# Performance work log

Measured on AMD Instinct MI355X. Metric: run time of the kernel, lower is better.

## Reference

```python
import jax, jax.numpy as jnp
import numpy as np
from jax import lax

EPS = 1e-5  # flax BatchNorm default epsilon


def _conv(x, w, b, padding='SAME'):
    y = lax.conv_general_dilated(x, w, (1, 1), padding,
                                 dimension_numbers=('NHWC', 'HWIO', 'NHWC'))
    return y + b


def _maxpool(x, window, strides):
    return lax.reduce_window(x, -jnp.inf, lax.max,
                             (1,) + window + (1,), (1,) + strides + (1,), 'SAME')


def _bn_train(x, scale, bias):
    # training-mode BatchNorm: batch statistics over N,H,W
    m = x.mean(axis=(0, 1, 2))
    v = x.var(axis=(0, 1, 2))
    return (x - m) * lax.rsqrt(v + EPS) * scale + bias


def _lstm(x, wx, wh, b, carry, reverse):
    # x: (B, T, D); flax LSTMCell gate order i, f, g, o; bias lives on the
    # hidden dense in flax but is an equivalent single additive term here.
    xs = jnp.swapaxes(x @ wx + b, 0, 1)  # (T, B, 4H), input GEMM hoisted out of scan

    def step(ch, xt):
        c, h = ch
        g = xt + h @ wh
        i, f, gg, o = jnp.split(g, 4, axis=-1)
        c = jax.nn.sigmoid(f) * c + jax.nn.sigmoid(i) * jnp.tanh(gg)
        h = jax.nn.sigmoid(o) * jnp.tanh(c)
        return (c, h), h

    carry, ys = lax.scan(step, carry, xs, reverse=reverse)
    return carry, jnp.swapaxes(ys, 0, 1)  # (B, T, H)


def _forward(x, conv1_w, conv1_b, conv2_w, conv2_b, conv3_w, conv3_b, bn1_s, bn1_b,
             conv4_w, conv4_b, bn2_s, bn2_b, conv5_w, conv5_b, bn3_s, bn3_b,
             conv6_w, conv6_b, bn4_s, bn4_b, conv7_w, conv7_b, bn5_s, bn5_b,
             wq, bq, wk, bk, wv, bv,
             l1f_wx, l1f_wh, l1f_b, l1r_wx, l1r_wh, l1r_b,
             l2f_wx, l2f_wh, l2f_b, l2r_wx, l2r_wh, l2r_b, wo, bo):
    x = jax.nn.relu(_conv(x, conv1_w, conv1_b))
    x = _maxpool(x, (2, 2), (2, 2))
    x = jax.nn.relu(_conv(x, conv2_w, conv2_b))
    x = _maxpool(x, (2, 2), (2, 2))
    x = jax.nn.relu(_bn_train(_conv(x, conv3_w, conv3_b), bn1_s, bn1_b))
    x = jax.nn.relu(_bn_train(_conv(x, conv4_w, conv4_b), bn2_s, bn2_b))
    x = _maxpool(x, (2, 2), (1, 2))
    x = jax.nn.relu(_bn_train(_conv(x, conv5_w, conv5_b), bn3_s, bn3_b))
    x = jax.nn.relu(_bn_train(_conv(x, conv6_w, conv6_b), bn4_s, bn4_b))
    x = _maxpool(x, (2, 2), (1, 2))
    x = jax.nn.relu(_bn_train(_conv(x, conv7_w, conv7_b, padding='VALID'), bn5_s, bn5_b))
    B = x.shape[0]
    x = x.reshape(B, x.shape[1], -1)  # (B, T=H', W'*512); seq axis is height
    q = x @ wq + bq
    k = x @ wk + bk
    v = x @ wv + bv
    qk = jax.nn.softmax(jnp.einsum('btk,bsk->bts', q, k) / 32.0, axis=-1)
    x = jnp.einsum('btk,bts->bsk', v, qk)
    # stack 1: reverse LSTM deliberately starts from forward's FINAL carry (as in source)
    carry = (jnp.zeros((B, 256), x.dtype), jnp.zeros((B, 256), x.dtype))
    carry, y1 = _lstm(x, l1f_wx, l1f_wh, l1f_b, carry, reverse=False)
    carry, y2 = _lstm(x, l1r_wx, l1r_wh, l1r_b, carry, reverse=True)
    x1 = jnp.concatenate([y1, y2], axis=-1)
    # stack 2
    carry = (jnp.zeros((B, 512), x.dtype), jnp.zeros((B, 512), x.dtype))
    carry, y2b = _lstm(x1, l2f_wx, l2f_wh, l2f_b, carry, reverse=False)
    carry, y3 = _lstm(x1, l2r_wx, l2r_wh, l2r_b, carry, reverse=True)
    x = jnp.concatenate([y3, y2b], axis=-1)
    return x @ wo + bo


def setup_inputs() -> dict:
    key = jax.random.key(0)
    ks = iter(jax.random.split(key, 64))

    def cw(kh, kw, ci, co):
        return jax.random.normal(next(ks), (kh, kw, ci, co), jnp.float32) / np.float32(np.sqrt(kh * kw * ci))

    def dw(i, o):
        return jax.random.normal(next(ks), (i, o), jnp.float32) / np.float32(np.sqrt(i))

    z = lambda *s: jnp.zeros(s, jnp.float32)
    ones = lambda *s: jnp.ones(s, jnp.float32)
    class_nums = 1000
    d_in = 15 * 512  # W'=15 after conv stack, 512 channels
    inp = {
        'x': jax.random.normal(next(ks), (32, 64, 256, 3), jnp.float32),
        'conv1_w': cw(3, 3, 3, 64), 'conv1_b': z(64),
        'conv2_w': cw(3, 3, 64, 128), 'conv2_b': z(128),
        'conv3_w': cw(3, 3, 128, 256), 'conv3_b': z(256), 'bn1_s': ones(256), 'bn1_b': z(256),
        'conv4_w': cw(3, 3, 256, 256), 'conv4_b': z(256), 'bn2_s': ones(256), 'bn2_b': z(256),
        'conv5_w': cw(3, 3, 256, 512), 'conv5_b': z(512), 'bn3_s': ones(512), 'bn3_b': z(512),
        'conv6_w': cw(3, 3, 512, 512), 'conv6_b': z(512), 'bn4_s': ones(512), 'bn4_b': z(512),
        'conv7_w': cw(2, 2, 512, 512), 'conv7_b': z(512), 'bn5_s': ones(512), 'bn5_b': z(512),
        'wq': dw(d_in, 512), 'bq': z(512),
        'wk': dw(d_in, 512), 'bk': z(512),
        'wv': dw(d_in, 512), 'bv': z(512),
        'l1f_wx': dw(512, 4 * 256), 'l1f_wh': dw(256, 4 * 256), 'l1f_b': z(4 * 256),
        'l1r_wx': dw(512, 4 * 256), 'l1r_wh': dw(256, 4 * 256), 'l1r_b': z(4 * 256),
        'l2f_wx': dw(512, 4 * 512), 'l2f_wh': dw(512, 4 * 512), 'l2f_b': z(4 * 512),
        'l2r_wx': dw(512, 4 * 512), 'l2r_wh': dw(512, 4 * 512), 'l2r_b': z(4 * 512),
        'wo': dw(1024, class_nums), 'bo': z(class_nums),
    }
    return inp


def reference(x, conv1_w, conv1_b, conv2_w, conv2_b, conv3_w, conv3_b, bn1_s, bn1_b,
              conv4_w, conv4_b, bn2_s, bn2_b, conv5_w, conv5_b, bn3_s, bn3_b,
              conv6_w, conv6_b, bn4_s, bn4_b, conv7_w, conv7_b, bn5_s, bn5_b,
              wq, bq, wk, bk, wv, bv,
              l1f_wx, l1f_wh, l1f_b, l1r_wx, l1r_wh, l1r_b,
              l2f_wx, l2f_wh, l2f_b, l2r_wx, l2r_wh, l2r_b, wo, bo):
    return _forward(x, conv1_w, conv1_b, conv2_w, conv2_b, conv3_w, conv3_b, bn1_s, bn1_b,
                    conv4_w, conv4_b, bn2_s, bn2_b, conv5_w, conv5_b, bn3_s, bn3_b,
                    conv6_w, conv6_b, bn4_s, bn4_b, conv7_w, conv7_b, bn5_s, bn5_b,
                    wq, bq, wk, bk, wv, bv,
                    l1f_wx, l1f_wh, l1f_b, l1r_wx, l1r_wh, l1r_b,
                    l2f_wx, l2f_wh, l2f_b, l2r_wx, l2r_wh, l2r_b, wo, bo)
```

## Files before the change

### kernel.cpp

```cpp
#include <hip/hip_runtime.h>
#include <math.h>

#define DIV_UP(a,b) (((a)+(b)-1)/(b))

typedef _Float16 half_t;
typedef _Float16 half8 __attribute__((ext_vector_type(8)));
typedef float f32x4 __attribute__((ext_vector_type(4)));

#define FLAG_RELU   1
#define FLAG_OUTF32 2
#define FLAG_SPLITK 4
#define FLAG_ATOMIC 8
#define FLAG_BNSUMS 16

#define GLDS16(src, dst) \
  __builtin_amdgcn_global_load_lds((const __attribute__((address_space(1))) void*)(src), \
                                   (__attribute__((address_space(3))) void*)(dst), 16, 0, 0)

__device__ __forceinline__ float fsig_(float x){ return 1.0f/(1.0f+__expf(-x)); }
__device__ __forceinline__ float ftanh_(float x){
  float ax = fabsf(x);
  float e = __expf(-2.0f*ax);
  float t = (1.0f - e)/(1.0f + e);
  return copysignf(t, x);
}

#define NTP 18
struct TpAll {
  const float* src[NTP];
  half_t* dst[NTP];
  int K[NTP];
  int N[NTP];
  int prefix[NTP+1];
};

__global__ __launch_bounds__(256) void transpose_cvt_all_kernel(TpAll a)
{
  __shared__ float tile[32][33];
  int bid = blockIdx.x;
  int z = 0;
  while (bid >= a.prefix[z+1]) ++z;
  int local = bid - a.prefix[z];
  const float* w = a.src[z];
  half_t* wT = a.dst[z];
  int K = a.K[z], N = a.N[z];
  int tilesX = (N + 31) >> 5;
  int nt = (local % tilesX) * 32;
  int kt = (local / tilesX) * 32;
  int tx = threadIdx.x & 31, ty = threadIdx.x >> 5;
  #pragma unroll
  for (int r = 0; r < 4; ++r) {
    int k = kt + ty + r*8, n = nt + tx;
    tile[ty + r*8][tx] = (k < K && n < N) ? w[(long)k*N + n] : 0.f;
  }
  __syncthreads();
  #pragma unroll
  for (int r = 0; r < 4; ++r) {
    int n = nt + ty + r*8, k = kt + tx;
    if (n < N && k < K) wT[(long)n*K + k] = (half_t)tile[tx][ty + r*8];
  }
}

__global__ __launch_bounds__(256) void conv1_kernel(
    const float* __restrict__ x, const float* __restrict__ w,
    const float* __restrict__ bias, half_t* __restrict__ out)
{
  __shared__ float xs[3][258*3];
  int nb = blockIdx.x;
  int n = nb >> 6, ho = nb & 63;
  int tid = threadIdx.x;
  int co = tid & 63;
  float wreg[27];
  #pragma unroll
  for (int k = 0; k < 27; ++k) wreg[k] = w[k*64 + co];
  float bco = bias[co];
  for (int i = tid; i < 3*258*3; i += 256) {
    int row = i / (258*3); int rem = i % (258*3);
    int col = rem / 3;     int ci  = rem % 3;
    int ih = ho - 1 + row; int iw = col - 1;
    float v = 0.f;
    if (ih >= 0 && ih < 64 && iw >= 0 && iw < 256)
      v = x[(((long)n*64 + ih)*256 + iw)*3 + ci];
    xs[row][col*3 + ci] = v;
  }
  __syncthreads();
  int wave = tid >> 6;
  for (int p = 0; p < 64; ++p) {
    int wo = wave*64 + p;
    float acc = bco;
    #pragma unroll
    for (int kh = 0; kh < 3; ++kh)
      #pragma unroll
      for (int kw = 0; kw < 3; ++kw)
        #pragma unroll
        for (int ci = 0; ci < 3; ++ci)
          acc = fmaf(xs[kh][(wo+kw)*3 + ci], wreg[(kh*3+kw)*3 + ci], acc);
    acc = fmaxf(acc, 0.f);
    out[(((long)n*64 + ho)*256 + wo)*64 + co] = (half_t)acc;
  }
}

struct GOut { const half_t* wT; const float* bias; void* out; };

__global__ __launch_bounds__(256) void mfma_conv_kernel(
    const half_t* __restrict__ x, GOut g0, GOut g1, GOut g2,
    const half_t* __restrict__ zbuf, float* __restrict__ bns,
    int N,int H,int W,int Ci,int Ho,int Wo,int Co,
    int KH,int KW,int padH,int padW,
    int M,int K,int flags,int splitS)
{
  GOut g;
  int ciBeg = 0, ciEnd = Ci;
  if (flags & FLAG_SPLITK) {
    g = g0;
    int span = Ci / splitS;
    ciBeg = blockIdx.z * span;
    ciEnd = ciBeg + span;
  } else {
    g = (blockIdx.z == 0) ? g0 : (blockIdx.z == 1 ? g1 : g2);
  }
  const half_t* __restrict__ wT = g.wT;
  __shared__ half_t As[2][128*64];
  __shared__ half_t Bs[2][128*64];
  int tid = threadIdx.x;

  int nbx = gridDim.x, nby = gridDim.y;
  int total = nbx * nby;
  int flat = blockIdx.y * nbx + blockIdx.x;
  int q = total >> 3, r = total & 7;
  int xcd = flat & 7;
  int j = flat >> 3;
  int w = xcd * q + (xcd < r ? xcd : r) + j;
  int m0 = (w / nbx) * 128, n0 = (w % nbx) * 128;

  int wave = tid >> 6, lane = tid & 63;
  int l15 = lane & 15, quad = lane >> 4;
  int x7 = lane & 7;
  int wm = (wave & 1) * 64, wn = (wave >> 1) * 64;

  int rSub = tid >> 3;
  int colHalf = (((tid & 7) ^ (rSub & 7))) * 8;

  int ho_[4], wo_[4], ni_[4]; bool av_[4];
  #pragma unroll
  for (int i = 0; i < 4; ++i) {
    int m = m0 + i*32 + rSub;
    av_[i] = m < M;
    int mm = av_[i] ? m : 0;
    wo_[i] = mm % Wo; int t2 = mm / Wo;
    ho_[i] = t2 % Ho; ni_[i] = t2 / Ho;
  }
  const half_t* bBase[4];
  #pragma unroll
  for (int i = 0; i < 4; ++i) {
    int n = n0 + i*32 + rSub;
    bBase[i] = (n < Co) ? (wT + (long)n*K + colHalf) : nullptr;
  }

  int pch0 = ((quad)     ^ x7) * 8;
  int pch1 = ((4 + quad) ^ x7) * 8;

  f32x4 acc[4][4];
  #pragma unroll
  for (int i = 0; i < 4; ++i)
    #pragma unroll
    for (int j2 = 0; j2 < 4; ++j2)
      acc[i][j2] = (f32x4){0.f, 0.f, 0.f, 0.f};

  int NT = ((ciEnd - ciBeg) >> 6) * KH * KW;
  int skh = 0, skw = 0, sci = ciBeg;
  long sAOff[4]; bool sAval[4];
  auto recompA = [&]() {
    #pragma unroll
    for (int i = 0; i < 4; ++i) {
      int ih = ho_[i] - padH + skh, iw = wo_[i] - padW + skw;
      bool ok = av_[i] && ih >= 0 && ih < H && iw >= 0 && iw < W;
      sAval[i] = ok;
      sAOff[i] = ok ? ((((long)ni_[i]*H + ih)*W + iw)*(long)Ci + colHalf) : 0;
    }
  };
  recompA();
  auto stage = [&](int b) {
    int kgS = (skh*KW + skw)*Ci + sci;
    #pragma unroll
    for (int i = 0; i < 4; ++i) {
      const half_t* sa = sAval[i] ? (x + sAOff[i] + sci) : zbuf;
      GLDS16(sa, &As[b][i*2048 + wave*512]);
      const half_t* sb = bBase[i] ? (bBase[i] + kgS) : zbuf;
      GLDS16(sb, &Bs[b][i*2048 + wave*512]);
    }
  };
  auto advance = [&]() {
    sci += 64;
    if (sci == ciEnd) {
      sci = ciBeg; ++skw;
      if (skw == KW) { skw = 0; ++skh; }
      recompA();
    }
  };

  stage(0); advance();
  __syncthreads();

  for (int kt = 0; kt < NT; ++kt) {
    int p = kt & 1;
    if (kt + 1 < NT) { stage(p ^ 1); advance(); }
    {
      half8 af[4], bf[4];
      #pragma unroll
      for (int i = 0; i < 4; ++i)
        af[i] = *reinterpret_cast<half8*>(&As[p][(wm + i*16 + l15)*64 + pch0]);
      #pragma unroll
      for (int j2 = 0; j2 < 4; ++j2)
        bf[j2] = *reinterpret_cast<half8*>(&Bs[p][(wn + j2*16 + l15)*64 + pch0]);
      #pragma unroll
      for (int i = 0; i < 4; ++i)
        #pragma unroll
        for (int j2 = 0; j2 < 4; ++j2)
          acc[i][j2] = __builtin_amdgcn_mfma_f32_16x16x32_f16(af[i], bf[j2], acc[i][j2], 0, 0, 0);
    }
    {
      half8 af[4], bf[4];
      #pragma unroll
      for (int i = 0; i < 4; ++i)
        af[i] = *reinterpret_cast<half8*>(&As[p][(wm + i*16 + l15)*64 + pch1]);
      #pragma unroll
      for (int j2 = 0; j2 < 4; ++j2)
        bf[j2] = *reinterpret_cast<half8*>(&Bs[p][(wn + j2*16 + l15)*64 + pch1]);
      #pragma unroll
      for (int i = 0; i < 4; ++i)
        #pragma unroll
        for (int j2 = 0; j2 < 4; ++j2)
          acc[i][j2] = __builtin_amdgcn_mfma_f32_16x16x32_f16(af[i], bf[j2], acc[i][j2], 0, 0, 0);
    }
    __syncthreads();
  }

  if (flags & FLAG_BNSUMS) {
    float* red = (float*)As;
    #pragma unroll
    for (int j2 = 0; j2 < 4; ++j2) {
      int n = n0 + wn + j2*16 + l15;
      float bv = g.bias[n];
      float s = 0.f, qq = 0.f;
      #pragma unroll
      for (int i = 0; i < 4; ++i)
        #pragma unroll
        for (int rr = 0; rr < 4; ++rr) {
          int m = m0 + wm + i*16 + quad*4 + rr;
          if (m < M) { float v = acc[i][j2][rr] + bv; s += v; qq += v*v; }
        }
      int idx = ((((wave*4 + quad)*16 + l15)*4) + j2)*2;
      red[idx] = s; red[idx+1] = qq;
    }
    __syncthreads();
    if (tid < 128) {
      int hi = tid >> 6;
      int jj = (tid >> 4) & 3, ll = tid & 15;
      float s = 0.f, qq = 0.f;
      #pragma unroll
      for (int w2 = 0; w2 < 2; ++w2)
        #pragma unroll
        for (int qd = 0; qd < 4; ++qd) {
          int idx = (((((hi*2 + w2)*4 + qd)*16 + ll)*4) + jj)*2;
          s += red[idx]; qq += red[idx+1];
        }
      int n = n0 + tid;
      atomicAdd(&bns[n], s);
      atomicAdd(&bns[Co + n], qq);
    }
  }

  #pragma unroll
  for (int i = 0; i < 4; ++i) {
    #pragma unroll
    for (int rr = 0; rr < 4; ++rr) {
      int m = m0 + wm + i*16 + quad*4 + rr;
      if (m >= M) continue;
      #pragma unroll
      for (int j2 = 0; j2 < 4; ++j2) {
        int n = n0 + wn + j2*16 + l15;
        if (n >= Co) continue;
        if (flags & FLAG_ATOMIC) {
          atomicAdd(&((float*)g.out)[(long)m*Co + n], acc[i][j2][rr]);
        } else {
          float v = acc[i][j2][rr] + g.bias[n];
          if (flags & FLAG_RELU) v = fmaxf(v, 0.f);
          if (flags & FLAG_OUTF32) ((float*)g.out)[(long)m*Co + n] = v;
          else ((half_t*)g.out)[(long)m*Co + n] = (half_t)v;
        }
      }
    }
  }
}

__global__ __launch_bounds__(256) void maxpool8_kernel(
    const half_t* __restrict__ x, half_t* __restrict__ out,
    int N,int H,int W,int C,int Ho,int Wo,int sH,int sW)
{
  int C8 = C >> 3;
  long idx = (long)blockIdx.x*256 + threadIdx.x;
  long total8 = (long)N*Ho*Wo*C8;
  if (idx >= total8) return;
  int cb = (int)(idx % C8);
  long pix = idx / C8;
  int wo = (int)(pix % Wo); long t2 = pix / Wo;
  int ho = (int)(t2 % Ho); int n = (int)(t2 / Ho);
  int c = cb * 8;
  float m[8];
  #pragma unroll
  for (int e = 0; e < 8; ++e) m[e] = -INFINITY;
  for (int i = 0; i < 2; ++i) {
    int ih = ho*sH + i;
    if (ih >= H) continue;
    for (int j = 0; j < 2; ++j) {
      int iw = wo*sW + j;
      if (iw >= W) continue;
      half8 v = *reinterpret_cast<const half8*>(x + (((long)n*H + ih)*W + iw)*C + c);
      #pragma unroll
      for (int e = 0; e < 8; ++e) m[e] = fmaxf(m[e], (float)v[e]);
    }
  }
  half8 o;
  #pragma unroll
  for (int e = 0; e < 8; ++e) o[e] = (half_t)m[e];
  *reinterpret_cast<half8*>(out + idx*8) = o;
}

__global__ __launch_bounds__(256) void bn_apply_relu8_kernel(
    half_t* __restrict__ x, const float* __restrict__ sums,
    const float* __restrict__ scale, const float* __restrict__ bias,
    long total8, int C, float invN)
{
  long idx = (long)blockIdx.x*256 + threadIdx.x;
  if (idx >= total8) return;
  int c = (int)((idx*8) % C);
  half8 v = *reinterpret_cast<half8*>(x + idx*8);
  half8 o;
  #pragma unroll
  for (int e = 0; e < 8; ++e) {
    float mean = sums[c+e] * invN;
    float var  = sums[C + c+e] * invN - mean*mean;
    float rstd = rsqrtf(var + 1e-5f);
    float y = ((float)v[e] - mean) * rstd * scale[c+e] + bias[c+e];
    o[e] = (half_t)fmaxf(y, 0.0f);
  }
  *reinterpret_cast<half8*>(x + idx*8) = o;
}

__global__ __launch_bounds__(256) void bn_pool8_kernel(
    const half_t* __restrict__ x, half_t* __restrict__ out,
    const float* __restrict__ sums, const float* __restrict__ scale,
    const float* __restrict__ bias,
    int N,int H,int W,int C,int Ho,int Wo,int sH,int sW, float invN)
{
  int C8 = C >> 3;
  long idx = (long)blockIdx.x*256 + threadIdx.x;
  long total8 = (long)N*Ho*Wo*C8;
  if (idx >= total8) return;
  int cb = (int)(idx % C8);
  long pix = idx / C8;
  int wo = (int)(pix % Wo); long t2 = pix / Wo;
  int ho = (int)(t2 % Ho); int n = (int)(t2 / Ho);
  int c = cb * 8;
  float mean[8], rs[8], bb[8];
  #pragma unroll
  for (int e = 0; e < 8; ++e) {
    mean[e] = sums[c+e] * invN;
    float var = sums[C + c+e] * invN - mean[e]*mean[e];
    rs[e] = rsqrtf(var + 1e-5f) * scale[c+e];
    bb[e] = bias[c+e];
  }
  float m[8];
  #pragma unroll
  for (int e = 0; e < 8; ++e) m[e] = -INFINITY;
  for (int i = 0; i < 2; ++i) {
    int ih = ho*sH + i;
    if (ih >= H) continue;
    for (int j = 0; j < 2; ++j) {
      int iw = wo*sW + j;
      if (iw >= W) continue;
      half8 v = *reinterpret_cast<const half8*>(x + (((long)n*H + ih)*W + iw)*C + c);
      #pragma unroll
      for (int e = 0; e < 8; ++e) {
        float y = fmaxf(((float)v[e] - mean[e]) * rs[e] + bb[e], 0.f);
        m[e] = fmaxf(m[e], y);
      }
    }
  }
  half8 o;
  #pragma unroll
  for (int e = 0; e < 8; ++e) o[e] = (half_t)m[e];
  *reinterpret_cast<half8*>(out + idx*8) = o;
}

__global__ __launch_bounds__(256) void bias_fill_kernel(
    float* __restrict__ out, const float* __restrict__ b0,
    const float* __restrict__ b1, const float* __restrict__ b2, int total)
{
  int idx = blockIdx.x*256 + threadIdx.x;
  if (idx >= total) return;
  int n = idx % 1536;
  float v = (n < 512) ? b0[n] : (n < 1024 ? b1[n-512] : b2[n-1024]);
  out[idx] = v;
}

__global__ __launch_bounds__(256) void attention_kernel(
    const float* __restrict__ qkv, half_t* __restrict__ out,
    int T, int D, int ld)
{
  int b = blockIdx.x;
  int tid = threadIdx.x;
  __shared__ float P[15][16];
  if (tid < T*T) {
    int t = tid / T, s = tid % T;
    const float* qp = qkv + ((long)b*T + t)*ld;
    const float* kp = qkv + ((long)b*T + s)*ld + 512;
    float acc = 0.f;
    for (int d = 0; d < D; d += 4) {
      float4 qv = *reinterpret_cast<const float4*>(qp + d);
      float4 kv = *reinterpret_cast<const float4*>(kp + d);
      acc += qv.x*kv.x + qv.y*kv.y + qv.z*kv.z + qv.w*kv.w;
    }
    P[t][s] = acc * (1.0f/32.0f);
  }
  __syncthreads();
  if (tid < T) {
    float mx = -INFINITY;
    for (int s = 0; s < T; ++s) mx = fmaxf(mx, P[tid][s]);
    float sum = 0.f;
    for (int s = 0; s < T; ++s) { float e = expf(P[tid][s] - mx); P[tid][s] = e; sum += e; }
    float inv = 1.0f / sum;
    for (int s = 0; s < T; ++s) P[tid][s] *= inv;
  }
  __syncthreads();
  for (int idx = tid; idx < T*D; idx += 256) {
    int s = idx / D, kk2 = idx % D;
    float acc = 0.f;
    #pragma unroll
    for (int t = 0; t < 15; ++t)
      acc += qkv[((long)b*T + t)*ld + 1024 + kk2] * P[t][s];
    out[((long)b*T + s)*D + kk2] = (half_t)acc;
  }
}

#define MAXK 512
#define HSROW (MAXK + 8)

template<int N64, int HLOG>
__device__ __forceinline__ void stage_h(
    const unsigned long long* __restrict__ src, half_t (*hs)[HSROW], int tid)
{
  unsigned long long tmp[N64];
  #pragma unroll
  for (int u = 0; u < N64; ++u)
    tmp[u] = __hip_atomic_load(src + tid + u*256, __ATOMIC_RELAXED, __HIP_MEMORY_SCOPE_AGENT);
  #pragma unroll
  for (int u = 0; u < N64; ++u) {
    int idx = tid + u*256;
    int row = idx >> (HLOG - 2);
    int col = (idx & ((1 << (HLOG - 2)) - 1)) * 4;
    *reinterpret_cast<unsigned long long*>(&hs[row][col]) = tmp[u];
  }
}

template<int H>
__global__ __launch_bounds__(256, 1) void lstm_persistent_kernel(
    const float* __restrict__ preF, const float* __restrict__ preR,
    const half_t* __restrict__ whTF, const half_t* __restrict__ whTR,
    half_t* __restrict__ hbuf, half_t* __restrict__ y,
    int* __restrict__ flags, int nblk,
    int ystride, int yoffF, int yoffR)
{
  constexpr int KI = H / 32;
  __shared__ half_t hs[32][HSROW];
  __shared__ float gates[32][133];
  int tid = threadIdx.x;
  int jb0 = blockIdx.x * 32;
  int lane = tid & 63, wave = tid >> 6;
  int l15 = lane & 15, quad = lane >> 4;
  int bb = tid >> 3;
  int jj0 = (tid & 7) * 4;
  constexpr int H4 = 4 * H;

  float cst[4] = {0.f, 0.f, 0.f, 0.f};
  half8 wreg[2][KI];

  auto loadw = [&](const half_t* __restrict__ whT) {
    #pragma unroll
    for (int f = 0; f < 2; ++f) {
      const half_t* wp = whT + (long)(wave*H + jb0 + f*16 + l15)*H + quad*8;
      #pragma unroll
      for (int i = 0; i < KI; ++i)
        wreg[f][i] = *reinterpret_cast<const half8*>(wp + i*32);
    }
  };

  auto loadpv = [&](int s, float (&pv)[16]) {
    const float* pr = (s < 15) ? preF : preR;
    int t = (s < 15) ? s : 29 - s;
    const float* pp = pr + (long)(bb*15 + t)*H4 + jb0 + jj0;
    #pragma unroll
    for (int g = 0; g < 4; ++g) {
      f32x4 v = *reinterpret_cast<const f32x4*>(pp + g*H);
      pv[g*4+0] = v[0]; pv[g*4+1] = v[1]; pv[g*4+2] = v[2]; pv[g*4+3] = v[3];
    }
  };

  loadw(whTF);
  float pv[16];
  loadpv(0, pv);

  for (int s = 0; s < 30; ++s) {
    if (s == 15) loadw(whTR);
    int t = (s < 15) ? s : 29 - s;
    int yoff = (s < 15) ? yoffF : yoffR;

    const unsigned long long* hsrc =
        (const unsigned long long*)(hbuf + (long)(s & 1) * 32 * H);
    if constexpr (H == 512) stage_h<16, 9>(hsrc, hs, tid);
    else                    stage_h<8, 8>(hsrc, hs, tid);
    __syncthreads();

    f32x4 acc00 = {0.f,0.f,0.f,0.f}, acc10 = {0.f,0.f,0.f,0.f};
    f32x4 acc01 = {0.f,0.f,0.f,0.f}, acc11 = {0.f,0.f,0.f,0.f};
    #pragma unroll
    for (int i = 0; i < KI; ++i) {
      half8 a0 = *reinterpret_cast<half8*>(&hs[l15][i*32 + quad*8]);
      half8 a1 = *reinterpret_cast<half8*>(&hs[16 + l15][i*32 + quad*8]);
      acc00 = __builtin_amdgcn_mfma_f32_16x16x32_f16(a0, wreg[0][i], acc00, 0, 0, 0);
      acc10 = __builtin_amdgcn_mfma_f32_16x16x32_f16(a1, wreg[0][i], acc10, 0, 0, 0);
      acc01 = __builtin_amdgcn_mfma_f32_16x16x32_f16(a0, wreg[1][i], acc01, 0, 0, 0);
      acc11 = __builtin_amdgcn_mfma_f32_16x16x32_f16(a1, wreg[1][i], acc11, 0, 0, 0);
    }
    #pragma unroll
    for (int r = 0; r < 4; ++r) {
      gates[quad*4 + r][wave*32 + l15]           = acc00[r];
      gates[16 + quad*4 + r][wave*32 + l15]      = acc10[r];
      gates[quad*4 + r][wave*32 + 16 + l15]      = acc01[r];
      gates[16 + quad*4 + r][wave*32 + 16 + l15] = acc11[r];
    }
    __syncthreads();

    unsigned long long hpack;
    {
      half_t hn[4];
      #pragma unroll
      for (int p = 0; p < 4; ++p) {
        int j = jj0 + p;
        float gi = pv[p]      + gates[bb][j];
        float gf = pv[4 + p]  + gates[bb][32 + j];
        float gg = pv[8 + p]  + gates[bb][64 + j];
        float go = pv[12 + p] + gates[bb][96 + j];
        gi = fsig_(gi); gf = fsig_(gf); gg = ftanh_(gg); go = fsig_(go);
        float cn = gf * cst[p] + gi * gg;
        cst[p] = cn;
        hn[p] = (half_t)(go * ftanh_(cn));
      }
      hpack = *reinterpret_cast<unsigned long long*>(hn);
      half_t* hdst = hbuf + (long)((s + 1) & 1) * 32 * H;
      __hip_atomic_store((unsigned long long*)(hdst + (long)bb*H + jb0 + jj0), hpack,
                         __ATOMIC_RELAXED, __HIP_MEMORY_SCOPE_AGENT);
    }

    if (s < 29) {
      __syncthreads();
      if (tid == 0)
        __hip_atomic_store(&flags[blockIdx.x], s + 1,
                           __ATOMIC_RELAXED, __HIP_MEMORY_SCOPE_AGENT);
      *reinterpret_cast<unsigned long long*>(
          &y[(long)(bb*15 + t)*ystride + yoff + jb0 + jj0]) = hpack;
      loadpv(s + 1, pv);
      if (tid < 64) {
        int target = s + 1;
        for (;;) {
          int vv = (tid < nblk)
            ? __hip_atomic_load(&flags[tid], __ATOMIC_RELAXED, __HIP_MEMORY_SCOPE_AGENT)
            : target;
          if (__all(vv >= target)) break;
        }
      }
      __syncthreads();
    } else {
      *reinterpret_cast<unsigned long long*>(
          &y[(long)(bb*15 + t)*ystride + yoff + jb0 + jj0]) = hpack;
    }
  }
}

extern "C" void kernel_launch(void* const* d_in, const int* in_sizes, int n_in,
                              void* d_out, int out_size, void* d_ws, size_t ws_size,
                              hipStream_t stream)
{
  const float* x       = (const float*)d_in[0];
  const float* c1w     = (const float*)d_in[1];  const float* c1b = (const float*)d_in[2];
  const float* c2w     = (const float*)d_in[3];  const float* c2b = (const float*)d_in[4];
  const float* c3w     = (const float*)d_in[5];  const float* c3b = (const float*)d_in[6];
  const float* bn1s    = (const float*)d_in[7];  const float* bn1b = (const float*)d_in[8];
  const float* c4w     = (const float*)d_in[9];  const float* c4b = (const float*)d_in[10];
  const float* bn2s    = (const float*)d_in[11]; const float* bn2b = (const float*)d_in[12];
  const float* c5w     = (const float*)d_in[13]; const float* c5b = (const float*)d_in[14];
  const float* bn3s    = (const float*)d_in[15]; const float* bn3b = (const float*)d_in[16];
  const float* c6w     = (const float*)d_in[17]; const float* c6b = (const float*)d_in[18];
  const float* bn4s    = (const float*)d_in[19]; const float* bn4b = (const float*)d_in[20];
  const float* c7w     = (const float*)d_in[21]; const float* c7b = (const float*)d_in[22];
  const float* bn5s    = (const float*)d_in[23]; const float* bn5b = (const float*)d_in[24];
  const float* wq      = (const float*)d_in[25]; const float* bq = (const float*)d_in[26];
  const float* wk      = (const float*)d_in[27]; const float* bk = (const float*)d_in[28];
  const float* wv      = (const float*)d_in[29]; const float* bv = (const float*)d_in[30];
  const float* l1f_wx  = (const float*)d_in[31]; const float* l1f_wh = (const float*)d_in[32]; const float* l1f_b = (const float*)d_in[33];
  const float* l1r_wx  = (const float*)d_in[34]; const float* l1r_wh = (const float*)d_in[35]; const float* l1r_b = (const float*)d_in[36];
  const float* l2f_wx  = (const float*)d_in[37]; const float* l2f_wh = (const float*)d_in[38]; const float* l2f_b = (const float*)d_in[39];
  const float* l2r_wx  = (const float*)d_in[40]; const float* l2r_wh = (const float*)d_in[41]; const float* l2r_b = (const float*)d_in[42];
  const float* wo      = (const float*)d_in[43]; const float* bo = (const float*)d_in[44];
  float* outp = (float*)d_out;

  char* base = (char*)d_ws;
  half_t* actA = (half_t*)base;
  half_t* actB = (half_t*)(base + 67108864);
  half_t* wtA  = (half_t*)(base + 100663296);
  float*  f32a = (float*)(base + 143687680);
  half_t* h16a = (half_t*)(base + 158736384);

  half_t* wt2  = wtA;
  half_t* wt3  = wtA + 73728;
  half_t* wt4  = wtA + 368640;
  half_t* wt5  = wtA + 958464;
  half_t* wt6  = wtA + 2138112;
  half_t* wt7  = wtA + 4497408;
  half_t* wtq  = wtA + 5545984;
  half_t* wtk  = wtA + 9478144;
  half_t* wtv  = wtA + 13410304;
  half_t* wt1f = wtA + 17342464;
  half_t* wt1r = wtA + 17866752;
  half_t* wt2f = wtA + 18391040;
  half_t* wt2r = wtA + 19439616;
  half_t* wto  = wtA + 20488192;

  float* qkvbuf = f32a;
  float* pre1f = f32a + 737280;
  float* pre1r = f32a + 1228800;
  float* pre2f = f32a + 1720320;
  float* pre2r = f32a + 2703360;

  half_t* ao  = h16a;
  half_t* x1  = h16a + 245760;
  half_t* x2  = h16a + 491520;
  half_t* hb1 = h16a + 983040;
  half_t* hb2 = hb1 + 16384;
  int*    flags1 = (int*)(hb2 + 32768);
  int*    flags2 = flags1 + 512;
  half_t* zbuf   = (half_t*)(flags2 + 512);
  float*  bnz    = (float*)(zbuf + 32);

  half_t* whT1f = (half_t*)(base + 160849920);
  half_t* whT1r = (half_t*)(base + 161374208);
  half_t* whT2f = (half_t*)(base + 161898496);
  half_t* whT2r = (half_t*)(base + 163995648);

  auto convm = [&](const half_t* in, const half_t* wt, const float* b, void* out,
                   int N,int H,int W,int Ci,int Ho,int Wo,int Co,
                   int KH,int KW,int pH,int pW,int flags, float* bns){
    int M = N*Ho*Wo, K = KH*KW*Ci;
    dim3 grid(DIV_UP(Co,128), DIV_UP(M,128), 1);
    GOut g{wt, b, out};
    mfma_conv_kernel<<<grid,256,0,stream>>>(in,g,g,g,zbuf,bns,N,H,W,Ci,Ho,Wo,Co,
                                            KH,KW,pH,pW,M,K,flags,1);
  };
  auto gemm3 = [&](const half_t* A, GOut g0, GOut g1, GOut g2, int nz,
                   int M, int Nn, int K, int flags, int splitS){
    dim3 grid(DIV_UP(Nn,128), DIV_UP(M,128), nz);
    mfma_conv_kernel<<<grid,256,0,stream>>>(A,g0,g1,g2,zbuf,bnz,M,1,1,K,1,1,Nn,
                                            1,1,0,0,M,K,flags,splitS);
  };
  auto pool = [&](const half_t* in, half_t* out, int N,int H,int W,int C,
                  int Ho,int Wo,int sH,int sW){
    long total8 = (long)N*Ho*Wo*(C/8);
    maxpool8_kernel<<<(int)DIV_UP(total8,256),256,0,stream>>>(in,out,N,H,W,C,Ho,Wo,sH,sW);
  };
  auto bnApply = [&](half_t* buf, long nPix, int C, const float* s, const float* b,
                     float* sums){
    long total8 = nPix * C / 8;
    bn_apply_relu8_kernel<<<(int)DIV_UP(total8,256),256,0,stream>>>(buf, sums, s, b, total8, C, 1.0f/(float)nPix);
  };
  auto bnPool = [&](const half_t* in, half_t* out, int N,int H,int W,int C,
                    int Ho,int Wo,int sH,int sW, long nPix,
                    const float* s, const float* b, float* sums){
    long total8 = (long)N*Ho*Wo*(C/8);
    bn_pool8_kernel<<<(int)DIV_UP(total8,256),256,0,stream>>>(
        in,out,sums,s,b,N,H,W,C,Ho,Wo,sH,sW,1.0f/(float)nPix);
  };

  hipMemsetAsync(hb1, 0, 143424, stream);

  {
    TpAll tp;
    const float* srcs[NTP] = {c2w,c3w,c4w,c5w,c6w,c7w,wq,wk,wv,l1f_wx,l1r_wx,l2f_wx,l2r_wx,wo,
                              l1f_wh,l1r_wh,l2f_wh,l2r_wh};
    half_t* dsts[NTP] = {wt2,wt3,wt4,wt5,wt6,wt7,wtq,wtk,wtv,wt1f,wt1r,wt2f,wt2r,wto,
                         whT1f,whT1r,whT2f,whT2r};
    int Ks[NTP] = {576,1152,2304,2304,4608,2048,7680,7680,7680,512,512,512,512,1024,
                   256,256,512,512};
    int Ns[NTP] = {128,256,256,512,512,512,512,512,512,1024,1024,2048,2048,1000,
                   1024,1024,2048,2048};
    int acc = 0;
    for (int i = 0; i < NTP; ++i) {
      tp.src[i] = srcs[i]; tp.dst[i] = dsts[i]; tp.K[i] = Ks[i]; tp.N[i] = Ns[i];
      tp.prefix[i] = acc;
      acc += DIV_UP(Ks[i],32) * DIV_UP(Ns[i],32);
    }
    tp.prefix[NTP] = acc;
    transpose_cvt_all_kernel<<<acc,256,0,stream>>>(tp);
  }

  conv1_kernel<<<2048,256,0,stream>>>(x, c1w, c1b, actA);
  pool(actA, actB, 32,64,256,64,  32,128, 2,2);
  convm(actB, wt2, c2b, actA, 32,32,128,64,  32,128,128, 3,3,1,1, FLAG_RELU, bnz);
  pool(actA, actB, 32,32,128,128, 16,64, 2,2);
  convm(actB, wt3, c3b, actA, 32,16,64,128,  16,64,256,  3,3,1,1, FLAG_BNSUMS, bnz);
  bnApply(actA, 32768, 256, bn1s, bn1b, bnz);
  convm(actA, wt4, c4b, actB, 32,16,64,256,  16,64,256,  3,3,1,1, FLAG_BNSUMS, bnz + 2048);
  bnPool(actB, actA, 32,16,64,256, 16,32, 1,2, 32768, bn2s, bn2b, bnz + 2048);
  convm(actA, wt5, c5b, actB, 32,16,32,256,  16,32,512,  3,3,1,1, FLAG_BNSUMS, bnz + 4096);
  bnApply(actB, 16384, 512, bn3s, bn3b, bnz + 4096);
  convm(actB, wt6, c6b, actA, 32,16,32,512,  16,32,512,  3,3,1,1, FLAG_BNSUMS, bnz + 6144);
  bnPool(actA, actB, 32,16,32,512, 16,16, 1,2, 16384, bn4s, bn4b, bnz + 6144);
  convm(actB, wt7, c7b, actA, 32,16,16,512,  15,15,512,  2,2,0,0, FLAG_BNSUMS, bnz + 8192);
  bnApply(actA, 7200, 512, bn5s, bn5b, bnz + 8192);

  bias_fill_kernel<<<DIV_UP(480*1536,256),256,0,stream>>>(qkvbuf, bq, bk, bv, 480*1536);
  gemm3(actA, GOut{wtq, nullptr, qkvbuf}, GOut{wtq, nullptr, qkvbuf},
        GOut{wtq, nullptr, qkvbuf}, 4, 480, 1536, 7680, FLAG_SPLITK|FLAG_ATOMIC, 4);
  attention_kernel<<<32,256,0,stream>>>(qkvbuf, ao, 15, 512, 1536);

  gemm3(ao, GOut{wt1f, l1f_b, pre1f}, GOut{wt1r, l1r_b, pre1r},
        GOut{wt1r, l1r_b, pre1r}, 2, 480, 1024, 512, FLAG_OUTF32, 1);
  lstm_persistent_kernel<256><<<8,256,0,stream>>>(
      pre1f, pre1r, whT1f, whT1r, hb1, x1, flags1, 8, 512, 0, 256);

  gemm3(x1, GOut{wt2f, l2f_b, pre2f}, GOut{wt2r, l2r_b, pre2r},
        GOut{wt2r, l2r_b, pre2r}, 2, 480, 2048, 512, FLAG_OUTF32, 1);
  lstm_persistent_kernel<512><<<16,256,0,stream>>>(
      pre2f, pre2r, whT2f, whT2r, hb2, x2, flags2, 16, 1024, 512, 0);

  gemm3(x2, GOut{wto, bo, outp}, GOut{wto, bo, outp}, GOut{wto, bo, outp}, 1,
        480, 1000, 1024, FLAG_OUTF32, 1);
}
```

Measured before the change: 1.041 ms.

## Read LSTM hidden state directly from global, spin per-wave, drop register weights

The persistent LSTM kernel no longer stages the shared hidden state into LDS or keeps recurrent weights in registers. Each wave now spins on the block flags itself at the top of the step, then reads h fragments straight from global memory with atomic loads and reloads weight fragments every step. This removes a block barrier and the LDS staging pass from the serial critical path. In exchange it adds global and L2 traffic for both h and weights on every timestep, and the relaxed-ordering synchronisation becomes subtler.

```diff
diff --git a/kernel.cpp b/kernel.cpp
--- a/kernel.cpp
+++ b/kernel.cpp
@@ -444,26 +444,6 @@
   }
 }
 
-#define MAXK 512
-#define HSROW (MAXK + 8)
-
-template<int N64, int HLOG>
-__device__ __forceinline__ void stage_h(
-    const unsigned long long* __restrict__ src, half_t (*hs)[HSROW], int tid)
-{
-  unsigned long long tmp[N64];
-  #pragma unroll
-  for (int u = 0; u < N64; ++u)
-    tmp[u] = __hip_atomic_load(src + tid + u*256, __ATOMIC_RELAXED, __HIP_MEMORY_SCOPE_AGENT);
-  #pragma unroll
-  for (int u = 0; u < N64; ++u) {
-    int idx = tid + u*256;
-    int row = idx >> (HLOG - 2);
-    int col = (idx & ((1 << (HLOG - 2)) - 1)) * 4;
-    *reinterpret_cast<unsigned long long*>(&hs[row][col]) = tmp[u];
-  }
-}
-
 template<int H>
 __global__ __launch_bounds__(256, 1) void lstm_persistent_kernel(
     const float* __restrict__ preF, const float* __restrict__ preR,
@@ -473,7 +453,6 @@
     int ystride, int yoffF, int yoffR)
 {
   constexpr int KI = H / 32;
-  __shared__ half_t hs[32][HSROW];
   __shared__ float gates[32][133];
   int tid = threadIdx.x;
   int jb0 = blockIdx.x * 32;
@@ -484,17 +463,11 @@
   constexpr int H4 = 4 * H;
 
   float cst[4] = {0.f, 0.f, 0.f, 0.f};
-  half8 wreg[2][KI];
-
-  auto loadw = [&](const half_t* __restrict__ whT) {
-    #pragma unroll
-    for (int f = 0; f < 2; ++f) {
-      const half_t* wp = whT + (long)(wave*H + jb0 + f*16 + l15)*H + quad*8;
-      #pragma unroll
-      for (int i = 0; i < KI; ++i)
-        wreg[f][i] = *reinterpret_cast<const half8*>(wp + i*32);
-    }
-  };
+
+  int o0 = l15 * (H >> 2) + quad * 2;
+  int o1 = (16 + l15) * (H >> 2) + quad * 2;
+
+  const half_t* wB = whTF;
 
   auto loadpv = [&](int s, float (&pv)[16]) {
     const float* pr = (s < 15) ? preF : preR;
@@ -507,31 +480,41 @@
     }
   };
 
-  loadw(whTF);
   float pv[16];
   loadpv(0, pv);
 
   for (int s = 0; s < 30; ++s) {
-    if (s == 15) loadw(whTR);
+    if (s == 15) wB = whTR;
     int t = (s < 15) ? s : 29 - s;
     int yoff = (s < 15) ? yoffF : yoffR;
 
-    const unsigned long long* hsrc =
+    for (;;) {
+      int fv = (lane < nblk)
+        ? __hip_atomic_load(&flags[lane], __ATOMIC_RELAXED, __HIP_MEMORY_SCOPE_AGENT)
+        : 0x7fffffff;
+      if (__all(fv >= s)) break;
+    }
+
+    const unsigned long long* hb =
         (const unsigned long long*)(hbuf + (long)(s & 1) * 32 * H);
-    if constexpr (H == 512) stage_h<16, 9>(hsrc, hs, tid);
-    else                    stage_h<8, 8>(hsrc, hs, tid);
-    __syncthreads();
+    const half_t* w0 = wB + (long)(wave*H + jb0 + l15)*H + quad*8;
+    const half_t* w1 = wB + (long)(wave*H + jb0 + 16 + l15)*H + quad*8;
 
     f32x4 acc00 = {0.f,0.f,0.f,0.f}, acc10 = {0.f,0.f,0.f,0.f};
     f32x4 acc01 = {0.f,0.f,0.f,0.f}, acc11 = {0.f,0.f,0.f,0.f};
     #pragma unroll
     for (int i = 0; i < KI; ++i) {
-      half8 a0 = *reinterpret_cast<half8*>(&hs[l15][i*32 + quad*8]);
-      half8 a1 = *reinterpret_cast<half8*>(&hs[16 + l15][i*32 + quad*8]);
-      acc00 = __builtin_amdgcn_mfma_f32_16x16x32_f16(a0, wreg[0][i], acc00, 0, 0, 0);
-      acc10 = __builtin_amdgcn_mfma_f32_16x16x32_f16(a1, wreg[0][i], acc10, 0, 0, 0);
-      acc01 = __builtin_amdgcn_mfma_f32_16x16x32_f16(a0, wreg[1][i], acc01, 0, 0, 0);
-      acc11 = __builtin_amdgcn_mfma_f32_16x16x32_f16(a1, wreg[1][i], acc11, 0, 0, 0);
+      union { unsigned long long u[2]; half8 v; } a0, a1;
+      a0.u[0] = __hip_atomic_load(hb + o0 + i*8,     __ATOMIC_RELAXED, __HIP_MEMORY_SCOPE_AGENT);
+      a0.u[1] = __hip_atomic_load(hb + o0 + i*8 + 1, __ATOMIC_RELAXED, __HIP_MEMORY_SCOPE_AGENT);
+      a1.u[0] = __hip_atomic_load(hb + o1 + i*8,     __ATOMIC_RELAXED, __HIP_MEMORY_SCOPE_AGENT);
+      a1.u[1] = __hip_atomic_load(hb + o1 + i*8 + 1, __ATOMIC_RELAXED, __HIP_MEMORY_SCOPE_AGENT);
+      half8 bf0 = *reinterpret_cast<const half8*>(w0 + i*32);
+      half8 bf1 = *reinterpret_cast<const half8*>(w1 + i*32);
+      acc00 = __builtin_amdgcn_mfma_f32_16x16x32_f16(a0.v, bf0, acc00, 0, 0, 0);
+      acc10 = __builtin_amdgcn_mfma_f32_16x16x32_f16(a1.v, bf0, acc10, 0, 0, 0);
+      acc01 = __builtin_amdgcn_mfma_f32_16x16x32_f16(a0.v, bf1, acc01, 0, 0, 0);
+      acc11 = __builtin_amdgcn_mfma_f32_16x16x32_f16(a1.v, bf1, acc11, 0, 0, 0);
     }
     #pragma unroll
     for (int r = 0; r < 4; ++r) {
@@ -571,16 +554,6 @@
       *reinterpret_cast<unsigned long long*>(
           &y[(long)(bb*15 + t)*ystride + yoff + jb0 + jj0]) = hpack;
       loadpv(s + 1, pv);
-      if (tid < 64) {
-        int target = s + 1;
-        for (;;) {
-          int vv = (tid < nblk)
-            ? __hip_atomic_load(&flags[tid], __ATOMIC_RELAXED, __HIP_MEMORY_SCOPE_AGENT)
-            : target;
-          if (__all(vv >= target)) break;
-        }
-      }
-      __syncthreads();
     } else {
       *reinterpret_cast<unsigned long long*>(
           &y[(long)(bb*15 + t)*ystride + yoff + jb0 + jj0]) = hpack;
```

Result: slower. 1.459 ms (+40.1%).

## Stream LSTM recurrent weights per step and let every wave spin on flags

Applied to the files above, without the earlier changes.

The persistent bidirectional LSTM kernel stops holding the recurrent weight fragments in registers. It now reloads them from global memory (likely L2-resident) inside the MFMA loop on every step. The inter-block barrier also changes: instead of wave 0 polling the flags followed by a __syncthreads, every wave polls the flag array itself at the start of the next step, which removes one block-wide barrier per step. This cuts register pressure and barrier latency but adds repeated weight reads on the serial recurrence critical path.

```diff
diff --git a/kernel.cpp b/kernel.cpp
--- a/kernel.cpp
+++ b/kernel.cpp
@@ -484,17 +484,8 @@
   constexpr int H4 = 4 * H;
 
   float cst[4] = {0.f, 0.f, 0.f, 0.f};
-  half8 wreg[2][KI];
-
-  auto loadw = [&](const half_t* __restrict__ whT) {
-    #pragma unroll
-    for (int f = 0; f < 2; ++f) {
-      const half_t* wp = whT + (long)(wave*H + jb0 + f*16 + l15)*H + quad*8;
-      #pragma unroll
-      for (int i = 0; i < KI; ++i)
-        wreg[f][i] = *reinterpret_cast<const half8*>(wp + i*32);
-    }
-  };
+
+  const half_t* wB = whTF;
 
   auto loadpv = [&](int s, float (&pv)[16]) {
     const float* pr = (s < 15) ? preF : preR;
@@ -507,14 +498,22 @@
     }
   };
 
-  loadw(whTF);
   float pv[16];
   loadpv(0, pv);
 
   for (int s = 0; s < 30; ++s) {
-    if (s == 15) loadw(whTR);
+    if (s == 15) wB = whTR;
     int t = (s < 15) ? s : 29 - s;
     int yoff = (s < 15) ? yoffF : yoffR;
+
+    if (s > 0) {
+      for (;;) {
+        int fv = (lane < nblk)
+          ? __hip_atomic_load(&flags[lane], __ATOMIC_RELAXED, __HIP_MEMORY_SCOPE_AGENT)
+          : 0x7fffffff;
+        if (__all(fv >= s)) break;
+      }
+    }
 
     const unsigned long long* hsrc =
         (const unsigned long long*)(hbuf + (long)(s & 1) * 32 * H);
@@ -522,16 +521,21 @@
     else                    stage_h<8, 8>(hsrc, hs, tid);
     __syncthreads();
 
+    const half_t* w0 = wB + (long)(wave*H + jb0 + l15)*H + quad*8;
+    const half_t* w1 = wB + (long)(wave*H + jb0 + 16 + l15)*H + quad*8;
+
     f32x4 acc00 = {0.f,0.f,0.f,0.f}, acc10 = {0.f,0.f,0.f,0.f};
     f32x4 acc01 = {0.f,0.f,0.f,0.f}, acc11 = {0.f,0.f,0.f,0.f};
     #pragma unroll
     for (int i = 0; i < KI; ++i) {
       half8 a0 = *reinterpret_cast<half8*>(&hs[l15][i*32 + quad*8]);
       half8 a1 = *reinterpret_cast<half8*>(&hs[16 + l15][i*32 + quad*8]);
-      acc00 = __builtin_amdgcn_mfma_f32_16x16x32_f16(a0, wreg[0][i], acc00, 0, 0, 0);
-      acc10 = __builtin_amdgcn_mfma_f32_16x16x32_f16(a1, wreg[0][i], acc10, 0, 0, 0);
-      acc01 = __builtin_amdgcn_mfma_f32_16x16x32_f16(a0, wreg[1][i], acc01, 0, 0, 0);
-      acc11 = __builtin_amdgcn_mfma_f32_16x16x32_f16(a1, wreg[1][i], acc11, 0, 0, 0);
+      half8 bf0 = *reinterpret_cast<const half8*>(w0 + i*32);
+      half8 bf1 = *reinterpret_cast<const half8*>(w1 + i*32);
+      acc00 = __builtin_amdgcn_mfma_f32_16x16x32_f16(a0, bf0, acc00, 0, 0, 0);
+      acc10 = __builtin_amdgcn_mfma_f32_16x16x32_f16(a1, bf0, acc10, 0, 0, 0);
+      acc01 = __builtin_amdgcn_mfma_f32_16x16x32_f16(a0, bf1, acc01, 0, 0, 0);
+      acc11 = __builtin_amdgcn_mfma_f32_16x16x32_f16(a1, bf1, acc11, 0, 0, 0);
     }
     #pragma unroll
     for (int r = 0; r < 4; ++r) {
@@ -571,16 +575,6 @@
       *reinterpret_cast<unsigned long long*>(
           &y[(long)(bb*15 + t)*ystride + yoff + jb0 + jj0]) = hpack;
       loadpv(s + 1, pv);
-      if (tid < 64) {
-        int target = s + 1;
-        for (;;) {
-          int vv = (tid < nblk)
-            ? __hip_atomic_load(&flags[tid], __ATOMIC_RELAXED, __HIP_MEMORY_SCOPE_AGENT)
-            : target;
-          if (__all(vv >= target)) break;
-        }
-      }
-      __syncthreads();
     } else {
       *reinterpret_cast<unsigned long long*>(
           &y[(long)(bb*15 + t)*ystride + yoff + jb0 + jj0]) = hpack;
```

Result: slower. 1.165 ms (+11.8%).
